# Optimization experiments

Hardware: AMD Instinct MI355X
Metric: run time of the kernel (lower is better)

Reference implementation:

```python
import jax, jax.numpy as jnp
import numpy as np

B, S, HID = 4, 1024, 4096
NH, NKV, HD = 32, 8, 128
FF = 11008
EPS = 1e-6
THETA = 10000.0


def rms_norm(x, w, eps=EPS):
    v = jnp.mean(jnp.square(x), axis=-1, keepdims=True)
    return x * jax.lax.rsqrt(v + eps) * w


def rotate_half(x):
    x1, x2 = jnp.split(x, 2, axis=-1)
    return jnp.concatenate([-x2, x1], axis=-1)


def rope_cos_sin(position_ids, head_dim=HD, theta=THETA):
    inv_freq = 1.0 / (theta ** (jnp.arange(0, head_dim, 2, dtype=jnp.float32) / head_dim))
    freqs = position_ids.astype(jnp.float32)[..., None] * inv_freq  # [B,S,HD/2]
    emb = jnp.concatenate([freqs, freqs], axis=-1)  # [B,S,HD]
    return jnp.cos(emb)[:, None, :, :], jnp.sin(emb)[:, None, :, :]  # [B,1,S,HD]


def setup_inputs() -> dict:
    key = jax.random.key(0)
    ks = jax.random.split(key, 9)
    sc = 0.02
    pos = jnp.tile(jnp.arange(S, dtype=jnp.int64 if jax.config.jax_enable_x64 else jnp.int32)[None, :], (B, 1))
    causal = jnp.tril(jnp.ones((S, S), dtype=bool))
    mask = jnp.where(causal, 0.0, -1e9).astype(jnp.float32)[None, None]  # [1,1,S,S]
    return {
        "hidden_states": jax.random.normal(ks[0], (B * S, HID), jnp.float32),
        "position_ids": pos,
        "attn_mask": mask,
        "Wq": jax.random.normal(ks[1], (HID, NH * HD), jnp.float32) * sc,
        "Wk": jax.random.normal(ks[2], (HID, NKV * HD), jnp.float32) * sc,
        "Wv": jax.random.normal(ks[3], (HID, NKV * HD), jnp.float32) * sc,
        "Wo": jax.random.normal(ks[4], (NH * HD, HID), jnp.float32) * sc,
        "ln1_w": jnp.ones((HID,), jnp.float32),
        "ln2_w": jnp.ones((HID,), jnp.float32),
        "w_gate": jax.random.normal(ks[5], (HID, FF), jnp.float32) * sc,
        "w_up": jax.random.normal(ks[6], (HID, FF), jnp.float32) * sc,
        "w_down": jax.random.normal(ks[7], (FF, HID), jnp.float32) * sc,
    }


def reference(hidden_states, position_ids, attn_mask, Wq, Wk, Wv, Wo, ln1_w, ln2_w, w_gate, w_up, w_down):
    residual = hidden_states
    h = rms_norm(hidden_states, ln1_w)

    # QKV projections on flat tokens, then reshape per train partition
    q = (h @ Wq).reshape(B, S, NH, HD).transpose(0, 2, 1, 3)     # [B,NH,S,HD]
    k = (h @ Wk).reshape(B, S, NKV, HD).transpose(0, 2, 1, 3)    # [B,NKV,S,HD]
    v = (h @ Wv).reshape(B, S, NKV, HD).transpose(0, 2, 1, 3)

    cos, sin = rope_cos_sin(position_ids)
    q = q * cos + rotate_half(q) * sin
    k = k * cos + rotate_half(k) * sin

    n_rep = NH // NKV
    k = jnp.repeat(k, n_rep, axis=1)  # [B,NH,S,HD]
    v = jnp.repeat(v, n_rep, axis=1)

    scores = jnp.einsum('bhqd,bhkd->bhqk', q, k) / np.sqrt(HD)
    scores = scores + attn_mask
    # softmax in fp32 as in the source
    probs = jax.nn.softmax(scores.astype(jnp.float32), axis=-1).astype(q.dtype)
    attn = jnp.einsum('bhqk,bhkd->bhqd', probs, v)               # [B,NH,S,HD]
    attn = attn.transpose(0, 2, 1, 3).reshape(B * S, NH * HD)
    h = attn @ Wo

    h = residual + h
    residual = h
    h2 = rms_norm(h, ln2_w)
    mlp = (jax.nn.silu(h2 @ w_gate) * (h2 @ w_up)) @ w_down
    return residual + mlp
```

## Files before the change

kernel.cpp:

```cpp
#include <hip/hip_runtime.h>

#define DEVINL __device__ __forceinline__

typedef unsigned short u16;
typedef __attribute__((ext_vector_type(8))) short bf16x8;
typedef __attribute__((ext_vector_type(4))) float f32x4;
typedef __attribute__((ext_vector_type(4))) unsigned short u16x4;


DEVINL float bf2f(u16 u) { union { unsigned i; float f; } x; x.i = ((unsigned)u) << 16; return x.f; }
DEVINL u16 f2bf(float f) {
  union { float f; unsigned i; } x; x.f = f;
  unsigned r = x.i + 0x7fffu + ((x.i >> 16) & 1u);
  return (u16)(r >> 16);
}

DEVINL void async16(u16* lds, const u16* g) {
  __builtin_amdgcn_global_load_lds((const __attribute__((address_space(1))) unsigned*)g,
                                   (__attribute__((address_space(3))) unsigned*)lds, 16, 0, 0);
}

__global__ __launch_bounds__(256) void conv_t(const float* __restrict__ in,
                                              u16* __restrict__ out, int K, int N) {
  __shared__ float tile[64][65];
  int k0 = blockIdx.y << 6, n0 = blockIdx.x << 6;
  int t = threadIdx.x;
  int r = t >> 4, c4 = (t & 15) << 2;
  #pragma unroll
  for (int it = 0; it < 4; it++) {
    int row = r + it*16;
    f32x4 v = *(const f32x4*)(in + (size_t)(k0 + row)*N + n0 + c4);
    tile[row][c4+0] = v[0]; tile[row][c4+1] = v[1];
    tile[row][c4+2] = v[2]; tile[row][c4+3] = v[3];
  }
  __syncthreads();
  #pragma unroll
  for (int it = 0; it < 4; it++) {
    int nrow = r + it*16;
    u16x4 ov;
    #pragma unroll
    for (int e = 0; e < 4; e++) ov[e] = f2bf(tile[c4+e][nrow]);
    *(u16x4*)(out + (size_t)(n0 + nrow)*K + k0 + c4) = ov;
  }
}

__global__ __launch_bounds__(256) void rmsnorm_kernel(const float* __restrict__ x,
                                                      const float* __restrict__ w,
                                                      u16* __restrict__ out) {
  int row = blockIdx.x, t = threadIdx.x;
  const float* xr = x + (size_t)row * 4096;
  f32x4 v[4];
  float ss = 0.f;
  #pragma unroll
  for (int i = 0; i < 4; i++) {
    v[i] = *(const f32x4*)(xr + (t + 256*i)*4);
    ss += v[i][0]*v[i][0] + v[i][1]*v[i][1] + v[i][2]*v[i][2] + v[i][3]*v[i][3];
  }
  #pragma unroll
  for (int d = 1; d < 64; d <<= 1) ss += __shfl_xor(ss, d, 64);
  __shared__ float ps[4];
  if ((t & 63) == 0) ps[t >> 6] = ss;
  __syncthreads();
  float scale = rsqrtf((ps[0]+ps[1]+ps[2]+ps[3]) * (1.f/4096.f) + 1e-6f);
  #pragma unroll
  for (int i = 0; i < 4; i++) {
    f32x4 wv = *(const f32x4*)(w + (t + 256*i)*4);
    u16x4 o;
    #pragma unroll
    for (int e = 0; e < 4; e++) o[e] = f2bf(v[i][e] * scale * wv[e]);
    *(u16x4*)(out + (size_t)row*4096 + (t + 256*i)*4) = o;
  }
}

__global__ __launch_bounds__(256) void rope_kernel(u16* __restrict__ q, u16* __restrict__ k) {
  int tok = blockIdx.x;
  int s = tok & 1023;
  __shared__ float cs[64], sn[64];
  int t = threadIdx.x;
  if (t < 64) {
    float inv = __expf(-(float)t * 0.14391156934f);
    float ang = (float)s * inv;
    cs[t] = cosf(ang); sn[t] = sinf(ang);
  }
  __syncthreads();
  const float qscale = 0.08838834764831845f;
  size_t qbase = (size_t)tok * 4096;
  #pragma unroll
  for (int it = 0; it < 8; it++) {
    int item = t + it*256; int h = item >> 6, j = item & 63;
    size_t i0 = qbase + h*128 + j;
    float x1 = bf2f(q[i0]), x2 = bf2f(q[i0+64]);
    float c = cs[j], si = sn[j];
    q[i0]    = f2bf((x1*c - x2*si) * qscale);
    q[i0+64] = f2bf((x2*c + x1*si) * qscale);
  }
  size_t kbase = (size_t)tok * 1024;
  #pragma unroll
  for (int it = 0; it < 2; it++) {
    int item = t + it*256; int h = item >> 6, j = item & 63;
    size_t i0 = kbase + h*128 + j;
    float x1 = bf2f(k[i0]), x2 = bf2f(k[i0+64]);
    float c = cs[j], si = sn[j];
    k[i0]    = f2bf(x1*c - x2*si);
    k[i0+64] = f2bf(x2*c + x1*si);
  }
}

__global__ __launch_bounds__(256) void vtrans(const u16* __restrict__ v, u16* __restrict__ vt) {
  __shared__ u16 tile[32][33];
  int bh = blockIdx.z; int b = bh >> 3, kvh = bh & 7;
  int d0 = blockIdx.x << 5, s0 = blockIdx.y << 5;
  int tx = threadIdx.x, ty = threadIdx.y;
  for (int r = ty; r < 32; r += 8)
    tile[r][tx] = v[(size_t)(b*1024 + s0 + r)*1024 + kvh*128 + d0 + tx];
  __syncthreads();
  for (int r = ty; r < 32; r += 8)
    vt[(size_t)((b*8 + kvh)*128 + d0 + r)*1024 + s0 + tx] = tile[tx][r];
}

template<int EPI>
__global__ __launch_bounds__(256, 2) void gemm_bt(
    const u16* __restrict__ A, const u16* __restrict__ Bt,
    void* __restrict__ Cv, const float* __restrict__ resid,
    const u16* __restrict__ gate, int M, int N, int K) {
  __shared__ u16 As[128*64];
  __shared__ u16 Bs[128*64];
  int nwg = gridDim.x;
  int bid = (int)blockIdx.x;
  int cpx = nwg >> 3;
  int swz = (bid & 7) * cpx + (bid >> 3);
  int mt = M >> 7;
  int m0 = (swz % mt) << 7;
  int n0 = (swz / mt) << 7;
  int tid = threadIdx.x;
  int lane = tid & 63, wave = tid >> 6;
  int wm = wave >> 1, wn = wave & 1;

  f32x4 acc[4][4];
  f32x4 zero = {0.f, 0.f, 0.f, 0.f};
  #pragma unroll
  for (int i = 0; i < 4; i++)
    #pragma unroll
    for (int j = 0; j < 4; j++) acc[i][j] = zero;

  int arow[4], acolb[4];
  #pragma unroll
  for (int i = 0; i < 4; i++) {
    int c = i*256 + tid;
    arow[i]  = c >> 3;
    acolb[i] = ((c & 7) * 16) ^ ((arow[i] & 7) << 4);
  }

  int nsteps = K >> 6;
  for (int t = 0; t < nsteps; t++) {
    int k0 = t << 6;
    #pragma unroll
    for (int i = 0; i < 4; i++) {
      async16(As + i*2048 + wave*512, A  + (size_t)(m0 + arow[i])*K + k0 + (acolb[i] >> 1));
      async16(Bs + i*2048 + wave*512, Bt + (size_t)(n0 + arow[i])*K + k0 + (acolb[i] >> 1));
    }
    __syncthreads();
    #pragma unroll
    for (int ks = 0; ks < 2; ks++) {
      bf16x8 af[4], bfr[4];
      int c2 = (ks*32 + (lane >> 4)*8) * 2;
      #pragma unroll
      for (int mf = 0; mf < 4; mf++) {
        int r = wm*64 + mf*16 + (lane & 15);
        af[mf] = *(const bf16x8*)(As + r*64 + ((c2 ^ ((r & 7) << 4)) >> 1));
      }
      #pragma unroll
      for (int nf = 0; nf < 4; nf++) {
        int r = wn*64 + nf*16 + (lane & 15);
        bfr[nf] = *(const bf16x8*)(Bs + r*64 + ((c2 ^ ((r & 7) << 4)) >> 1));
      }
      #pragma unroll
      for (int mf = 0; mf < 4; mf++)
        #pragma unroll
        for (int nf = 0; nf < 4; nf++)
          acc[mf][nf] = __builtin_amdgcn_mfma_f32_16x16x32_bf16(af[mf], bfr[nf], acc[mf][nf], 0, 0, 0);
    }
    __syncthreads();
  }

  #pragma unroll
  for (int mf = 0; mf < 4; mf++)
    #pragma unroll
    for (int nf = 0; nf < 4; nf++)
      #pragma unroll
      for (int j = 0; j < 4; j++) {
        int rr = m0 + wm*64 + mf*16 + (lane >> 4)*4 + j;
        int cc = n0 + wn*64 + nf*16 + (lane & 15);
        size_t idx = (size_t)rr * N + cc;
        float v = acc[mf][nf][j];
        if constexpr (EPI == 0) {
          ((u16*)Cv)[idx] = f2bf(v);
        } else if constexpr (EPI == 1) {
          ((float*)Cv)[idx] = v + resid[idx];
        } else {
          float g = bf2f(gate[idx]);
          float sg = g / (1.f + __expf(-g));
          ((u16*)Cv)[idx] = f2bf(sg * v);
        }
      }
}

#define SB0() __builtin_amdgcn_sched_barrier(0)
#define MFMAQ2(qm, qn, afr, bq) do { \
  _Pragma("unroll") for (int mf_ = 0; mf_ < 4; mf_++) \
  _Pragma("unroll") for (int nf_ = 0; nf_ < 2; nf_++) \
  _Pragma("unroll") for (int ks_ = 0; ks_ < 2; ks_++) \
    acc[(qm)*4+mf_][(qn)*2+nf_] = __builtin_amdgcn_mfma_f32_16x16x32_bf16( \
        afr[mf_][ks_], bq[nf_][ks_], acc[(qm)*4+mf_][(qn)*2+nf_], 0, 0, 0); \
} while (0)

template<int EPI>
__global__ __launch_bounds__(512, 2) void gemm256(
    const u16* __restrict__ A, const u16* __restrict__ Bt,
    void* __restrict__ Cv, const float* __restrict__ resid,
    const u16* __restrict__ gate, int M, int N, int K) {
  extern __shared__ u16 lds[];
  int nwg = gridDim.x, bid = (int)blockIdx.x;
  int cpx = nwg >> 3;
  int swz = (bid & 7) * cpx + (bid >> 3);
  int mt = M >> 8;
  int m0 = (swz % mt) << 8;
  int n0 = (swz / mt) << 8;
  int tid = threadIdx.x, lane = tid & 63, wave = tid >> 6;
  int wm = wave >> 2, wn = wave & 3;

  f32x4 acc[8][4];
  f32x4 zero = {0.f, 0.f, 0.f, 0.f};
  #pragma unroll
  for (int i = 0; i < 8; i++)
    #pragma unroll
    for (int j = 0; j < 4; j++) acc[i][j] = zero;

  int sgrow = lane >> 3;
  int sgcol = ((lane & 7) ^ (lane >> 3)) << 3;
  const u16* gA = A  + (size_t)(m0 + wave*8 + sgrow) * K + sgcol;
  const u16* gB = Bt + (size_t)(n0 + wave*8 + sgrow) * K + sgcol;
  size_t K64 = (size_t)64 * K, K128 = (size_t)128 * K, K192 = (size_t)192 * K;

  int rA = lane & 15;
  int sw = rA & 7;
  int acol0 = (((lane >> 4)    ) ^ sw) << 3;
  int acol1 = (((lane >> 4) + 4) ^ sw) << 3;

  bf16x8 af[4][2], b0[2][2], b1[2][2];

  auto stageA = [&](int kb, int k0) {
    u16* d = lds + kb*32768 + wave*512;
    const u16* s = gA + k0;
    async16(d,         s);
    async16(d + 4096,  s + K64);
    async16(d + 8192,  s + K128);
    async16(d + 12288, s + K192);
  };
  auto stageB = [&](int kb, int k0) {
    u16* d = lds + kb*32768 + 16384 + wave*512;
    const u16* s = gB + k0;
    async16(d,         s);
    async16(d + 4096,  s + K64);
    async16(d + 8192,  s + K128);
    async16(d + 12288, s + K192);
  };
  auto loadA = [&](int kb, int qm) {
    const u16* base = lds + kb*32768 + (wm*128 + qm*64 + rA)*64;
    #pragma unroll
    for (int mf = 0; mf < 4; mf++) {
      af[mf][0] = *(const bf16x8*)(base + mf*1024 + acol0);
      af[mf][1] = *(const bf16x8*)(base + mf*1024 + acol1);
    }
  };
  auto loadB = [&](int kb, int qn, bf16x8 (&bq)[2][2]) {
    const u16* base = lds + kb*32768 + 16384 + (wn*64 + qn*32 + rA)*64;
    #pragma unroll
    for (int nf = 0; nf < 2; nf++) {
      bq[nf][0] = *(const bf16x8*)(base + nf*1024 + acol0);
      bq[nf][1] = *(const bf16x8*)(base + nf*1024 + acol1);
    }
  };

  int nt = K >> 6;
  stageA(0, 0); stageB(0, 0);
  if (nt > 1) { stageA(1, 64); stageB(1, 64); }
  SB0();
  if (nt > 1) asm volatile("s_waitcnt vmcnt(8)" ::: "memory");
  else        asm volatile("s_waitcnt vmcnt(0)" ::: "memory");
  SB0();
  __builtin_amdgcn_s_barrier();

  for (int k = 0; k < nt; k++) {
    int kb = k & 1;
    bool pre = (k + 2) < nt;
    int k2 = (k + 2) << 6;
    loadA(kb, 0); loadB(kb, 0, b0); loadB(kb, 1, b1);
    SB0();
    __builtin_amdgcn_s_setprio(1);
    MFMAQ2(0, 0, af, b0);
    MFMAQ2(0, 1, af, b1);
    __builtin_amdgcn_s_setprio(0);
    loadA(kb, 1);
    SB0();
    asm volatile("s_waitcnt lgkmcnt(0)" ::: "memory");
    SB0();
    __builtin_amdgcn_s_barrier();
    if (pre) { stageB(kb, k2); stageA(kb, k2); }
    SB0();
    __builtin_amdgcn_s_setprio(1);
    MFMAQ2(1, 0, af, b0);
    MFMAQ2(1, 1, af, b1);
    __builtin_amdgcn_s_setprio(0);
    SB0();
    if (pre) asm volatile("s_waitcnt vmcnt(8)" ::: "memory");
    else     asm volatile("s_waitcnt vmcnt(0)" ::: "memory");
    SB0();
    __builtin_amdgcn_s_barrier();
  }

  #pragma unroll
  for (int mf = 0; mf < 8; mf++)
    #pragma unroll
    for (int nf = 0; nf < 4; nf++)
      #pragma unroll
      for (int j = 0; j < 4; j++) {
        int rr = m0 + wm*128 + mf*16 + (lane >> 4)*4 + j;
        int cc = n0 + wn*64 + nf*16 + (lane & 15);
        size_t idx = (size_t)rr * N + cc;
        float v = acc[mf][nf][j];
        if constexpr (EPI == 0) {
          ((u16*)Cv)[idx] = f2bf(v);
        } else if constexpr (EPI == 1) {
          ((float*)Cv)[idx] = v + resid[idx];
        } else {
          float g = bf2f(gate[idx]);
          float sg = g / (1.f + __expf(-g));
          ((u16*)Cv)[idx] = f2bf(sg * v);
        }
      }
}

__global__ __launch_bounds__(256, 2) void attn_kernel(
    const u16* __restrict__ q, const u16* __restrict__ k,
    const u16* __restrict__ vt, u16* __restrict__ out) {
  __shared__ u16 Ks[64*128];
  __shared__ u16 Vs[128*64];
  __shared__ u16 Ps[4*16*64];
  int bid = blockIdx.x;
  int qt = bid & 15;
  int h  = (bid >> 4) & 31;
  int b  = bid >> 9;
  int kvh = h >> 2;
  int tid = threadIdx.x, lane = tid & 63, wave = tid >> 6;
  int q0 = qt << 6;

  bf16x8 qf[4];
  {
    const u16* qb_ = q + (size_t)(b*1024 + q0 + wave*16 + (lane & 15))*4096 + h*128 + (lane >> 4)*8;
    #pragma unroll
    for (int ks = 0; ks < 4; ks++) qf[ks] = *(const bf16x8*)(qb_ + ks*32);
  }
  f32x4 o[8];
  f32x4 zero = {0.f,0.f,0.f,0.f};
  #pragma unroll
  for (int i = 0; i < 8; i++) o[i] = zero;
  float m[4] = {-1e30f,-1e30f,-1e30f,-1e30f};
  float l[4] = {0.f,0.f,0.f,0.f};

  int kr[4], kc[4], vr[4], vc[4];
  #pragma unroll
  for (int i = 0; i < 4; i++) {
    int c = i*256 + tid;
    kr[i] = c >> 4; kc[i] = ((c & 15)*16) ^ ((kr[i] & 7) << 4);
    vr[i] = c >> 3; vc[i] = ((c & 7)*16)  ^ ((vr[i] & 7) << 4);
  }

  for (int t = 0; t <= qt; t++) {
    int kv0 = t << 6;
    #pragma unroll
    for (int i = 0; i < 4; i++) {
      async16(Ks + i*2048 + wave*512, k  + (size_t)(b*1024 + kv0 + kr[i])*1024 + kvh*128 + (kc[i] >> 1));
      async16(Vs + i*2048 + wave*512, vt + (size_t)((b*8 + kvh)*128 + vr[i])*1024 + kv0 + (vc[i] >> 1));
    }
    __syncthreads();

    f32x4 s[4];
    #pragma unroll
    for (int nf = 0; nf < 4; nf++) {
      s[nf] = zero;
      #pragma unroll
      for (int ks = 0; ks < 4; ks++) {
        int r = nf*16 + (lane & 15);
        int c2 = (ks*32 + (lane >> 4)*8)*2;
        bf16x8 kf = *(const bf16x8*)(Ks + r*128 + ((c2 ^ ((r & 7) << 4)) >> 1));
        s[nf] = __builtin_amdgcn_mfma_f32_16x16x32_bf16(qf[ks], kf, s[nf], 0, 0, 0);
      }
    }
    if (t == qt) {
      #pragma unroll
      for (int nf = 0; nf < 4; nf++)
        #pragma unroll
        for (int j = 0; j < 4; j++) {
          int cc = nf*16 + (lane & 15);
          int rr = wave*16 + (lane >> 4)*4 + j;
          if (cc > rr) s[nf][j] = -1e30f;
        }
    }
    #pragma unroll
    for (int j = 0; j < 4; j++) {
      float mx = fmaxf(fmaxf(s[0][j], s[1][j]), fmaxf(s[2][j], s[3][j]));
      #pragma unroll
      for (int d = 1; d < 16; d <<= 1) mx = fmaxf(mx, __shfl_xor(mx, d, 64));
      float mn = fmaxf(m[j], mx);
      float f = __expf(m[j] - mn);
      m[j] = mn;
      float ssum = 0.f;
      #pragma unroll
      for (int nf = 0; nf < 4; nf++) {
        float p = __expf(s[nf][j] - mn);
        s[nf][j] = p; ssum += p;
      }
      #pragma unroll
      for (int d = 1; d < 16; d <<= 1) ssum += __shfl_xor(ssum, d, 64);
      l[j] = l[j]*f + ssum;
      #pragma unroll
      for (int nf = 0; nf < 8; nf++) o[nf][j] *= f;
    }
    #pragma unroll
    for (int nf = 0; nf < 4; nf++)
      #pragma unroll
      for (int j = 0; j < 4; j++) {
        int rr = (lane >> 4)*4 + j;
        int cb = ((nf*16 + (lane & 15))*2) ^ ((rr & 7) << 4);
        Ps[wave*1024 + rr*64 + (cb >> 1)] = f2bf(s[nf][j]);
      }
    #pragma unroll
    for (int ks2 = 0; ks2 < 2; ks2++) {
      int mr = lane & 15;
      int c2 = (ks2*32 + (lane >> 4)*8)*2;
      bf16x8 pa = *(const bf16x8*)(Ps + wave*1024 + mr*64 + ((c2 ^ ((mr & 7) << 4)) >> 1));
      #pragma unroll
      for (int nf = 0; nf < 8; nf++) {
        int d = nf*16 + (lane & 15);
        bf16x8 vf = *(const bf16x8*)(Vs + d*64 + ((c2 ^ ((d & 7) << 4)) >> 1));
        o[nf] = __builtin_amdgcn_mfma_f32_16x16x32_bf16(pa, vf, o[nf], 0, 0, 0);
      }
    }
    __syncthreads();
  }

  float inv[4];
  #pragma unroll
  for (int j = 0; j < 4; j++) inv[j] = 1.f / l[j];
  u16* ob = out + (size_t)(b*1024 + q0 + wave*16)*4096 + h*128;
  #pragma unroll
  for (int nf = 0; nf < 8; nf++)
    #pragma unroll
    for (int j = 0; j < 4; j++) {
      int rr = (lane >> 4)*4 + j;
      int cc = nf*16 + (lane & 15);
      ob[(size_t)rr*4096 + cc] = f2bf(o[nf][j] * inv[j]);
    }
}

extern "C" void kernel_launch(void* const* d_in, const int* in_sizes, int n_in,
                              void* d_out, int out_size, void* d_ws, size_t ws_size,
                              hipStream_t stream) {
  (void)in_sizes; (void)n_in; (void)out_size;
  const float* hidden = (const float*)d_in[0];
  const float* Wq  = (const float*)d_in[3];
  const float* Wk  = (const float*)d_in[4];
  const float* Wv  = (const float*)d_in[5];
  const float* Wo  = (const float*)d_in[6];
  const float* ln1 = (const float*)d_in[7];
  const float* ln2 = (const float*)d_in[8];
  const float* Wg  = (const float*)d_in[9];
  const float* Wu  = (const float*)d_in[10];
  const float* Wd  = (const float*)d_in[11];
  float* out = (float*)d_out;

  char* ws = (char*)d_ws;
  size_t off = 0;
  auto alloc = [&](size_t b) { char* p = ws + off; off += (b + 4095) & ~(size_t)4095; return p; };
  u16*  W1   = (u16*)alloc(90177536);
  u16*  h1   = (u16*)alloc(33554432);
  u16*  qb   = (u16*)alloc(33554432);
  u16*  kb   = (u16*)alloc(8388608);
  u16*  vb   = (u16*)alloc(8388608);
  u16*  vtb  = (u16*)alloc(8388608);
  float* hmid = (float*)alloc(67108864);
  u16*  gb   = (u16*)alloc(90177536);
  if (off > ws_size) return;

  u16* wqT = W1;
  u16* wkT = W1 + 16777216;
  u16* wvT = wkT + 4194304;

  hipFuncSetAttribute((const void*)gemm256<0>, hipFuncAttributeMaxDynamicSharedMemorySize, 131072);
  hipFuncSetAttribute((const void*)gemm256<1>, hipFuncAttributeMaxDynamicSharedMemorySize, 131072);
  hipFuncSetAttribute((const void*)gemm256<2>, hipFuncAttributeMaxDynamicSharedMemorySize, 131072);

  dim3 blk(256);
  conv_t<<<dim3(64, 64),  blk, 0, stream>>>(Wq, wqT, 4096, 4096);
  conv_t<<<dim3(16, 64),  blk, 0, stream>>>(Wk, wkT, 4096, 1024);
  conv_t<<<dim3(16, 64),  blk, 0, stream>>>(Wv, wvT, 4096, 1024);
  rmsnorm_kernel<<<4096, blk, 0, stream>>>(hidden, ln1, h1);
  gemm256<0><<<256, 512, 131072, stream>>>(h1, wqT, qb, nullptr, nullptr, 4096, 4096, 4096);
  gemm_bt<0><<<256, blk, 0, stream>>>(h1, wkT, kb, nullptr, nullptr, 4096, 1024, 4096);
  gemm_bt<0><<<256, blk, 0, stream>>>(h1, wvT, vb, nullptr, nullptr, 4096, 1024, 4096);
  rope_kernel<<<4096, blk, 0, stream>>>(qb, kb);
  vtrans<<<dim3(4, 32, 32), dim3(32, 8), 0, stream>>>(vb, vtb);
  attn_kernel<<<2048, blk, 0, stream>>>(qb, kb, vtb, h1);
  conv_t<<<dim3(64, 64), blk, 0, stream>>>(Wo, W1, 4096, 4096);
  gemm256<1><<<256, 512, 131072, stream>>>(h1, W1, hmid, hidden, nullptr, 4096, 4096, 4096);
  rmsnorm_kernel<<<4096, blk, 0, stream>>>(hmid, ln2, qb);
  conv_t<<<dim3(172, 64), blk, 0, stream>>>(Wg, W1, 4096, 11008);
  gemm256<0><<<688, 512, 131072, stream>>>(qb, W1, gb, nullptr, nullptr, 4096, 11008, 4096);
  conv_t<<<dim3(172, 64), blk, 0, stream>>>(Wu, W1, 4096, 11008);
  gemm256<2><<<688, 512, 131072, stream>>>(qb, W1, gb, nullptr, gb, 4096, 11008, 4096);
  conv_t<<<dim3(64, 172), blk, 0, stream>>>(Wd, W1, 11008, 4096);
  gemm256<1><<<256, 512, 131072, stream>>>(gb, W1, out, hmid, nullptr, 4096, 4096, 11008);
}
```

Before: 1.811 ms.

## Restructure 256x256 GEMM mainloop into quadrant-staged ping-pong pipeline

The bf16 GEMM mainloop now stages global-to-LDS loads per quadrant (A halves and B halves, two 16-byte loads each) into the alternate buffer one k-step ahead, instead of staging full tiles two steps ahead. Each quarter of the MFMA work is paired with its own LDS fragment reads, an async prefetch, a barrier and a tuned vmcnt wait. This changes the LDS tile layout so each quadrant is contiguous. The aim is finer interleaving of memory traffic with MFMA issue, at the cost of more barriers per iteration and a shallower prefetch distance.

```diff
diff --git a/kernel.cpp b/kernel.cpp
--- a/kernel.cpp
+++ b/kernel.cpp
@@ -206,13 +206,16 @@
 }
 
 #define SB0() __builtin_amdgcn_sched_barrier(0)
+#define MIDBAR() do { SB0(); __builtin_amdgcn_s_barrier(); \
+  asm volatile("s_waitcnt lgkmcnt(0)" ::: "memory"); SB0(); } while (0)
 #define MFMAQ2(qm, qn, afr, bq) do { \
+  __builtin_amdgcn_s_setprio(1); \
   _Pragma("unroll") for (int mf_ = 0; mf_ < 4; mf_++) \
   _Pragma("unroll") for (int nf_ = 0; nf_ < 2; nf_++) \
   _Pragma("unroll") for (int ks_ = 0; ks_ < 2; ks_++) \
     acc[(qm)*4+mf_][(qn)*2+nf_] = __builtin_amdgcn_mfma_f32_16x16x32_bf16( \
         afr[mf_][ks_], bq[nf_][ks_], acc[(qm)*4+mf_][(qn)*2+nf_], 0, 0, 0); \
-} while (0)
+  __builtin_amdgcn_s_setprio(0); } while (0)
 
 template<int EPI>
 __global__ __launch_bounds__(512, 2) void gemm256(
@@ -236,45 +239,39 @@
     #pragma unroll
     for (int j = 0; j < 4; j++) acc[i][j] = zero;
 
-  int sgrow = lane >> 3;
-  int sgcol = ((lane & 7) ^ (lane >> 3)) << 3;
-  const u16* gA = A  + (size_t)(m0 + wave*8 + sgrow) * K + sgcol;
-  const u16* gB = Bt + (size_t)(n0 + wave*8 + sgrow) * K + sgcol;
-  size_t K64 = (size_t)64 * K, K128 = (size_t)128 * K, K192 = (size_t)192 * K;
+  int sCol = ((lane & 7) ^ (lane >> 3)) << 3;
+  int aRow = ((wave >> 2)*128) + (wave & 3)*16 + (lane >> 3);
+  int bRow = ((wave >> 1)*64)  + (wave & 1)*16 + (lane >> 3);
+  const u16* gA = A  + (size_t)(m0 + aRow) * K + sCol;
+  const u16* gB = Bt + (size_t)(n0 + bRow) * K + sCol;
+  size_t K8 = (size_t)8 * K, K32 = (size_t)32 * K, K64 = (size_t)64 * K;
 
   int rA = lane & 15;
-  int sw = rA & 7;
-  int acol0 = (((lane >> 4)    ) ^ sw) << 3;
-  int acol1 = (((lane >> 4) + 4) ^ sw) << 3;
+  int acol0 = (((lane >> 4)    ) ^ (rA & 7)) << 3;
+  int acol1 = (((lane >> 4) + 4) ^ (rA & 7)) << 3;
 
   bf16x8 af[4][2], b0[2][2], b1[2][2];
 
-  auto stageA = [&](int kb, int k0) {
-    u16* d = lds + kb*32768 + wave*512;
-    const u16* s = gA + k0;
-    async16(d,         s);
-    async16(d + 4096,  s + K64);
-    async16(d + 8192,  s + K128);
-    async16(d + 12288, s + K192);
+  auto stageAq = [&](int buf, int qm, int k0) {
+    u16* d = lds + buf*32768 + qm*8192 + wave*1024;
+    const u16* s = gA + (size_t)qm*K64 + k0;
+    async16(d, s); async16(d + 512, s + K8);
   };
-  auto stageB = [&](int kb, int k0) {
-    u16* d = lds + kb*32768 + 16384 + wave*512;
-    const u16* s = gB + k0;
-    async16(d,         s);
-    async16(d + 4096,  s + K64);
-    async16(d + 8192,  s + K128);
-    async16(d + 12288, s + K192);
+  auto stageBq = [&](int buf, int qn, int k0) {
+    u16* d = lds + buf*32768 + 16384 + qn*8192 + wave*1024;
+    const u16* s = gB + (size_t)qn*K32 + k0;
+    async16(d, s); async16(d + 512, s + K8);
   };
-  auto loadA = [&](int kb, int qm) {
-    const u16* base = lds + kb*32768 + (wm*128 + qm*64 + rA)*64;
+  auto loadAq = [&](int buf, int qm) {
+    const u16* base = lds + buf*32768 + qm*8192 + wm*4096 + rA*64;
     #pragma unroll
     for (int mf = 0; mf < 4; mf++) {
       af[mf][0] = *(const bf16x8*)(base + mf*1024 + acol0);
       af[mf][1] = *(const bf16x8*)(base + mf*1024 + acol1);
     }
   };
-  auto loadB = [&](int kb, int qn, bf16x8 (&bq)[2][2]) {
-    const u16* base = lds + kb*32768 + 16384 + (wn*64 + qn*32 + rA)*64;
+  auto loadBq = [&](int buf, int qn, bf16x8 (&bq)[2][2]) {
+    const u16* base = lds + buf*32768 + 16384 + qn*8192 + wn*2048 + rA*64;
     #pragma unroll
     for (int nf = 0; nf < 2; nf++) {
       bq[nf][0] = *(const bf16x8*)(base + nf*1024 + acol0);
@@ -283,40 +280,43 @@
   };
 
   int nt = K >> 6;
-  stageA(0, 0); stageB(0, 0);
-  if (nt > 1) { stageA(1, 64); stageB(1, 64); }
+  stageAq(0, 0, 0); stageBq(0, 0, 0); stageBq(0, 1, 0); stageAq(0, 1, 0);
   SB0();
-  if (nt > 1) asm volatile("s_waitcnt vmcnt(8)" ::: "memory");
-  else        asm volatile("s_waitcnt vmcnt(0)" ::: "memory");
+  asm volatile("s_waitcnt vmcnt(4)" ::: "memory");
   SB0();
   __builtin_amdgcn_s_barrier();
 
   for (int k = 0; k < nt; k++) {
-    int kb = k & 1;
-    bool pre = (k + 2) < nt;
-    int k2 = (k + 2) << 6;
-    loadA(kb, 0); loadB(kb, 0, b0); loadB(kb, 1, b1);
+    int buf = k & 1, nbuf = buf ^ 1;
+    bool pre = (k + 1) < nt;
+    int k1 = (k + 1) << 6;
+    loadAq(buf, 0); loadBq(buf, 0, b0);
+    if (pre) stageAq(nbuf, 0, k1);
+    MIDBAR();
+    MFMAQ2(0, 0, af, b0);
     SB0();
-    __builtin_amdgcn_s_setprio(1);
-    MFMAQ2(0, 0, af, b0);
+    if (pre) asm volatile("s_waitcnt vmcnt(4)" ::: "memory");
+    else     asm volatile("s_waitcnt vmcnt(2)" ::: "memory");
+    SB0(); __builtin_amdgcn_s_barrier();
+    loadBq(buf, 1, b1);
+    if (pre) stageBq(nbuf, 0, k1);
+    MIDBAR();
     MFMAQ2(0, 1, af, b1);
-    __builtin_amdgcn_s_setprio(0);
-    loadA(kb, 1);
     SB0();
-    asm volatile("s_waitcnt lgkmcnt(0)" ::: "memory");
+    if (pre) asm volatile("s_waitcnt vmcnt(4)" ::: "memory");
+    else     asm volatile("s_waitcnt vmcnt(0)" ::: "memory");
+    SB0(); __builtin_amdgcn_s_barrier();
+    loadAq(buf, 1);
+    if (pre) stageBq(nbuf, 1, k1);
+    MIDBAR();
+    MFMAQ2(1, 0, af, b0);
+    SB0(); __builtin_amdgcn_s_barrier();
+    if (pre) stageAq(nbuf, 1, k1);
+    MIDBAR();
+    MFMAQ2(1, 1, af, b1);
     SB0();
-    __builtin_amdgcn_s_barrier();
-    if (pre) { stageB(kb, k2); stageA(kb, k2); }
-    SB0();
-    __builtin_amdgcn_s_setprio(1);
-    MFMAQ2(1, 0, af, b0);
-    MFMAQ2(1, 1, af, b1);
-    __builtin_amdgcn_s_setprio(0);
-    SB0();
-    if (pre) asm volatile("s_waitcnt vmcnt(8)" ::: "memory");
-    else     asm volatile("s_waitcnt vmcnt(0)" ::: "memory");
-    SB0();
-    __builtin_amdgcn_s_barrier();
+    if (pre) asm volatile("s_waitcnt vmcnt(4)" ::: "memory");
+    SB0(); __builtin_amdgcn_s_barrier();
   }
 
   #pragma unroll
```

After: 1.836 ms. No clear change (+1.4%).
